# Optimization experiments

Hardware: AMD Instinct MI355X
Metric: run time of the kernel (lower is better)

Reference implementation:

```python
import jax, jax.numpy as jnp
import numpy as np

B, N = 16, 512            # graphs per batch, nodes per graph
V, D_EMB = 100000, 64     # embedding table
F0 = 64                   # raw node feature width
H = 8                     # heads per layer
F_IN0 = F0 + D_EMB + 3    # 131 after concat(emb)+concat(user_emb)
O1, O2 = 128, 128         # f_out of layer 0 and 1
F_IN1 = H * O1            # 1024
EPS = 1e-5


def _xavier(key, shape):
    fan_in, fan_out = shape[-2], shape[-1]
    lim = float(np.sqrt(6.0 / (fan_in + fan_out)))
    return jax.random.uniform(key, shape, jnp.float32, -lim, lim)


def setup_inputs() -> dict:
    key = jax.random.key(0)
    ks = jax.random.split(key, 16)
    vertices = jax.random.randint(ks[0], (B, N), 0, V)
    adj = (jax.random.uniform(ks[1], (B, N, N)) < 0.1).astype(jnp.float32)
    adj = jnp.maximum(adj, jnp.eye(N, dtype=jnp.float32))  # self-loops: no empty softmax rows
    h = jax.random.normal(ks[2], (B, N, F0), jnp.float32)
    user_emb = jax.random.normal(ks[3], (B, N, 3), jnp.float32)
    emb_table = jax.random.normal(ks[4], (V, D_EMB), jnp.float32)
    return {
        "vertices": vertices, "adj": adj, "h": h, "user_emb": user_emb,
        "emb_table": emb_table,
        "norm1_w": jnp.ones((D_EMB,), jnp.float32), "norm1_b": jnp.zeros((D_EMB,), jnp.float32),
        "norm2_w": jnp.ones((3,), jnp.float32), "norm2_b": jnp.zeros((3,), jnp.float32),
        "w0": _xavier(ks[5], (H, F_IN0, O1)),
        "a_src0": _xavier(ks[6], (H, O1, 1)), "a_dst0": _xavier(ks[7], (H, O1, 1)),
        "w1": _xavier(ks[8], (H, F_IN1, O2)),
        "a_src1": _xavier(ks[9], (H, O2, 1)), "a_dst1": _xavier(ks[10], (H, O2, 1)),
    }


def _instance_norm(x, w, b):
    # torch InstanceNorm1d on x.transpose(1,2): normalize over node dim per (batch, channel)
    mu = jnp.mean(x, axis=1, keepdims=True)
    var = jnp.var(x, axis=1, keepdims=True)  # biased variance, as torch
    return (x - mu) * jax.lax.rsqrt(var + EPS) * w + b


def _gat_layer(h, adj, w, a_src, a_dst):
    # h: [b,n,f_in], w: [h,f_in,o]
    hp = jnp.einsum('bnf,hfo->bhno', h, w)            # h_prime
    t = jnp.tanh(hp)
    s = jnp.einsum('bhno,ho->bhn', t, a_src[..., 0])  # attn_src
    d = jnp.einsum('bhno,ho->bhn', t, a_dst[..., 0])  # attn_dst
    attn = s[:, :, :, None] + d[:, :, None, :]        # [b,h,n,n]
    attn = jnp.where(attn >= 0, attn, 0.2 * attn)     # leaky_relu(0.2)
    attn = jnp.where(adj[:, None, :, :] > 0, attn, -jnp.inf)
    attn = jax.nn.softmax(attn, axis=-1)              # (dropout is identity in eval)
    return jnp.einsum('bhnm,bhmo->bhno', attn, hp)


def reference(vertices, adj, h, user_emb, emb_table,
              norm1_w, norm1_b, norm2_w, norm2_b,
              w0, a_src0, a_dst0, w1, a_src1, a_dst1):
    emb = emb_table[vertices]                         # [b,n,D_EMB]
    emb = _instance_norm(emb, norm1_w, norm1_b)
    x = jnp.concatenate([h, emb], axis=2)
    ue = _instance_norm(user_emb, norm2_w, norm2_b)
    x = jnp.concatenate([x, ue], axis=2)              # [b,n,F_IN0]
    # layer 0 (not last): elu + head concat
    x = _gat_layer(x, adj, w0, a_src0, a_dst0)        # [b,H,n,O1]
    x = jax.nn.elu(jnp.transpose(x, (0, 2, 1, 3)).reshape(B, N, H * O1))
    # layer 1 (last): mean over heads
    x = _gat_layer(x, adj, w1, a_src1, a_dst1)        # [b,H,n,O2]
    x = jnp.mean(x, axis=1)                           # [b,n,O2]
    return jax.nn.log_softmax(x, axis=-1)
```

## Files before the change

### kernel.cpp

```cpp
#include <hip/hip_runtime.h>
#include <hip/hip_bf16.h>
#include <cmath>

#define B_  16
#define N_  512
#define H_  8
#define F0_ 64
#define DEMB_ 64
#define FIN0_ 131
#define KP0_ 192
#define O_  128
#define FIN1_ 1024

typedef __attribute__((ext_vector_type(4))) float f32x4;
typedef __attribute__((ext_vector_type(8))) short bf16x8;

__device__ inline ushort f2bf(float f) {
    union { float f; unsigned u; } x; x.f = f;
    unsigned r = x.u + 0x7fff + ((x.u >> 16) & 1);
    return (ushort)(r >> 16);
}
__device__ inline float bf2f(ushort u) {
    union { unsigned u; float f; } x; x.u = ((unsigned)u) << 16;
    return x.f;
}
__device__ inline float tanh_fast(float x) {
    x = fminf(fmaxf(x, -15.f), 15.f);
    float e = __expf(2.f * x);
    return (e - 1.f) * __frcp_rn(e + 1.f);
}

__global__ __launch_bounds__(256) void k_copy_h(const float* __restrict__ h,
                                                ushort* __restrict__ x0) {
    int i = blockIdx.x * 256 + threadIdx.x;
    int r = i >> 6, c = i & 63;
    x0[(size_t)r * KP0_ + c] = f2bf(h[i]);
    x0[(size_t)r * KP0_ + 128 + c] = 0;
}

__global__ __launch_bounds__(256) void k_emb_norm(const int* __restrict__ verts,
                                                  const float* __restrict__ table,
                                                  const float* __restrict__ w,
                                                  const float* __restrict__ bb,
                                                  ushort* __restrict__ x0) {
    int b = blockIdx.x >> 6, c = blockIdx.x & 63;
    int t = threadIdx.x;
    float vals[2], sum = 0.f, sq = 0.f;
#pragma unroll
    for (int i = 0; i < 2; ++i) {
        int n = t + i * 256;
        int vid = verts[b * N_ + n];
        float v = table[(size_t)vid * DEMB_ + c];
        vals[i] = v; sum += v; sq += v * v;
    }
    __shared__ float s0[256], s1[256];
    s0[t] = sum; s1[t] = sq; __syncthreads();
    for (int o = 128; o > 0; o >>= 1) {
        if (t < o) { s0[t] += s0[t + o]; s1[t] += s1[t + o]; }
        __syncthreads();
    }
    float mu = s0[0] * (1.f / N_);
    float var = s1[0] * (1.f / N_) - mu * mu;
    float inv = rsqrtf(var + 1e-5f);
    float ww = w[c], bv = bb[c];
#pragma unroll
    for (int i = 0; i < 2; ++i) {
        int n = t + i * 256;
        x0[((size_t)b * N_ + n) * KP0_ + 64 + c] = f2bf((vals[i] - mu) * inv * ww + bv);
    }
}

__global__ __launch_bounds__(256) void k_ue_norm(const float* __restrict__ ue,
                                                 const float* __restrict__ w,
                                                 const float* __restrict__ bb,
                                                 ushort* __restrict__ x0) {
    int b = blockIdx.x / 3, c = blockIdx.x % 3;
    int t = threadIdx.x;
    float vals[2], sum = 0.f, sq = 0.f;
#pragma unroll
    for (int i = 0; i < 2; ++i) {
        int n = t + i * 256;
        float v = ue[((size_t)b * N_ + n) * 3 + c];
        vals[i] = v; sum += v; sq += v * v;
    }
    __shared__ float s0[256], s1[256];
    s0[t] = sum; s1[t] = sq; __syncthreads();
    for (int o = 128; o > 0; o >>= 1) {
        if (t < o) { s0[t] += s0[t + o]; s1[t] += s1[t + o]; }
        __syncthreads();
    }
    float mu = s0[0] * (1.f / N_);
    float var = s1[0] * (1.f / N_) - mu * mu;
    float inv = rsqrtf(var + 1e-5f);
    float ww = w[c], bv = bb[c];
#pragma unroll
    for (int i = 0; i < 2; ++i) {
        int n = t + i * 256;
        x0[((size_t)b * N_ + n) * KP0_ + 128 + c] = f2bf((vals[i] - mu) * inv * ww + bv);
    }
}

template <int K, int Kp>
__global__ __launch_bounds__(128) void k_wt(const float* __restrict__ w,
                                            ushort* __restrict__ wt) {
    int hh = blockIdx.x / (Kp / 8);
    int kc = blockIdx.x % (Kp / 8);
    int o = threadIdx.x;
    bf16x8 v;
#pragma unroll
    for (int j = 0; j < 8; ++j) {
        int k = kc * 8 + j;
        float f = (k < K) ? w[((size_t)hh * K + k) * 128 + o] : 0.f;
        v[j] = (short)f2bf(f);
    }
    *(bf16x8*)(wt + ((size_t)(hh * 128 + o)) * Kp + kc * 8) = v;
}

__global__ __launch_bounds__(256) void k_mask(const float* __restrict__ adj,
                                              unsigned long long* __restrict__ mask) {
    int gid = blockIdx.x * 256 + threadIdx.x;
    float v = adj[gid];
    unsigned long long m = __ballot(v > 0.f);
    if ((threadIdx.x & 63) == 0) mask[gid >> 6] = m;
}

template <int K>
__global__ __launch_bounds__(256) void k_gemm(const ushort* __restrict__ A,
                                              const ushort* __restrict__ Wt,
                                              const float* __restrict__ asrc,
                                              const float* __restrict__ adst,
                                              ushort* __restrict__ hpT,
                                              float* __restrict__ sout,
                                              float* __restrict__ dout) {
    __shared__ ushort As[128 * 64];
    __shared__ ushort Bs[128 * 64];
    int bid = blockIdx.x;
    int hh = bid & 7;
    int mt = bid >> 3;
    int tid = threadIdx.x;
    int wid = tid >> 6, l = tid & 63;
    int wm = wid >> 1, wn = wid & 1;

    const ushort* Ab = A + (size_t)mt * 128 * K;
    const ushort* Wb = Wt + (size_t)hh * 128 * K;

    f32x4 acc[4][4];
#pragma unroll
    for (int m = 0; m < 4; ++m)
#pragma unroll
        for (int n = 0; n < 4; ++n) acc[m][n] = (f32x4){0.f, 0.f, 0.f, 0.f};

    int srow = tid >> 3;
    int segp = tid & 7;

    for (int kt = 0; kt < K / 64; ++kt) {
        int k0 = kt * 64;
#pragma unroll
        for (int it = 0; it < 4; ++it) {
            int row = it * 32 + srow;
            int segl = segp ^ (row & 7);
            __builtin_amdgcn_global_load_lds(
                (const __attribute__((address_space(1))) void*)(Ab + (size_t)row * K + k0 + segl * 8),
                (__attribute__((address_space(3))) void*)(As + (it * 32 + wid * 8) * 64),
                16, 0, 0);
            __builtin_amdgcn_global_load_lds(
                (const __attribute__((address_space(1))) void*)(Wb + (size_t)row * K + k0 + segl * 8),
                (__attribute__((address_space(3))) void*)(Bs + (it * 32 + wid * 8) * 64),
                16, 0, 0);
        }
        __syncthreads();

        int lr = l & 15;
        int kg = l >> 4;
#pragma unroll
        for (int kk = 0; kk < 2; ++kk) {
            int segl = kk * 4 + kg;
            bf16x8 a[4], b[4];
#pragma unroll
            for (int m = 0; m < 4; ++m) {
                int row = wm * 64 + m * 16 + lr;
                int sp = segl ^ (row & 7);
                a[m] = *(const bf16x8*)(As + row * 64 + sp * 8);
            }
#pragma unroll
            for (int n = 0; n < 4; ++n) {
                int row = wn * 64 + n * 16 + lr;
                int sp = segl ^ (row & 7);
                b[n] = *(const bf16x8*)(Bs + row * 64 + sp * 8);
            }
#pragma unroll
            for (int m = 0; m < 4; ++m)
#pragma unroll
                for (int n = 0; n < 4; ++n)
                    acc[m][n] = __builtin_amdgcn_mfma_f32_16x16x32_bf16(a[m], b[n], acc[m][n], 0, 0, 0);
        }
        __syncthreads();
    }

    int bb = mt >> 2;
    int n_in_b = (mt & 3) * 128;
    int bh = bb * H_ + hh;
    ushort* Hp = hpT + ((size_t)bh * 128) * 512;
#pragma unroll
    for (int m = 0; m < 4; ++m)
#pragma unroll
        for (int n = 0; n < 4; ++n) {
            int rr = wm * 64 + m * 16 + (l >> 4) * 4;
            int cc = wn * 64 + n * 16 + (l & 15);
            ushort4 v;
            v.x = f2bf(acc[m][n][0]);
            v.y = f2bf(acc[m][n][1]);
            v.z = f2bf(acc[m][n][2]);
            v.w = f2bf(acc[m][n][3]);
            *(ushort4*)(Hp + (size_t)cc * 512 + n_in_b + rr) = v;
        }

    float* sP = (float*)As;
    float* dP = sP + 256;
    float av[4], dv[4];
#pragma unroll
    for (int n = 0; n < 4; ++n) {
        int cc = wn * 64 + n * 16 + (l & 15);
        av[n] = asrc[hh * 128 + cc];
        dv[n] = adst[hh * 128 + cc];
    }
#pragma unroll
    for (int m = 0; m < 4; ++m)
#pragma unroll
        for (int j = 0; j < 4; ++j) {
            float sv = 0.f, dvv = 0.f;
#pragma unroll
            for (int n = 0; n < 4; ++n) {
                float th = tanh_fast(acc[m][n][j]);
                sv += th * av[n];
                dvv += th * dv[n];
            }
#pragma unroll
            for (int off = 1; off < 16; off <<= 1) {
                sv += __shfl_xor(sv, off);
                dvv += __shfl_xor(dvv, off);
            }
            if ((l & 15) == 0) {
                int rr = wm * 64 + m * 16 + (l >> 4) * 4 + j;
                sP[wn * 128 + rr] = sv;
                dP[wn * 128 + rr] = dvv;
            }
        }
    __syncthreads();
    if (tid < 128) {
        sout[(size_t)bh * 512 + n_in_b + tid] = sP[tid] + sP[128 + tid];
    } else {
        int r = tid - 128;
        dout[(size_t)bh * 512 + n_in_b + r] = dP[r] + dP[128 + r];
    }
}

template <bool L0>
__global__ __launch_bounds__(256, 2) void k_attn(const ushort* __restrict__ hpT,
                                                 const float* __restrict__ sbuf,
                                                 const float* __restrict__ dbuf,
                                                 const unsigned* __restrict__ mask32,
                                                 ushort* __restrict__ out) {
    __shared__ ushort Vbuf[128 * 64];
    __shared__ ushort Abuf[128 * 64];
    __shared__ float dsh[512];
    __shared__ float rsh[128];

    int bid = blockIdx.x;
    int xcd = bid & 7, idx = bid >> 3;
    int bh = xcd + 8 * (idx & 15);
    int tile = idx >> 4;
    int b = bh >> 3, hh = bh & 7;
    int n0 = tile * 128;
    int t = threadIdx.x;
    int wid = t >> 6, l = t & 63;
    int wm = wid >> 1, wn = wid & 1;
    int lr = l & 15, kg = l >> 4;

    const ushort* Vb = hpT + (size_t)bh * 128 * 512;

    int row = t >> 1, mh = t & 1;
    float sv = sbuf[(size_t)bh * 512 + n0 + row];
    unsigned mw[8];
#pragma unroll
    for (int c = 0; c < 8; ++c)
        mw[c] = mask32[((size_t)(b * 512 + n0 + row) << 4) + c * 2 + mh];

    dsh[t] = dbuf[(size_t)bh * 512 + t];
    dsh[256 + t] = dbuf[(size_t)bh * 512 + 256 + t];
    __syncthreads();

    f32x4 acc[4][4];
#pragma unroll
    for (int m = 0; m < 4; ++m)
#pragma unroll
        for (int n = 0; n < 4; ++n) acc[m][n] = (f32x4){0.f, 0.f, 0.f, 0.f};

    float rsum = 0.f;
    int srow = t >> 3, segp = t & 7;

    for (int c = 0; c < 8; ++c) {
        int m0 = c * 64;
#pragma unroll
        for (int it = 0; it < 4; ++it) {
            int rrow = it * 32 + srow;
            int segl = segp ^ (rrow & 7);
            __builtin_amdgcn_global_load_lds(
                (const __attribute__((address_space(1))) void*)(Vb + (size_t)rrow * 512 + m0 + segl * 8),
                (__attribute__((address_space(3))) void*)(Vbuf + (it * 32 + wid * 8) * 64),
                16, 0, 0);
        }

        const float* dp = dsh + m0 + mh * 32;
        unsigned mwc = mw[c];
#pragma unroll
        for (int j = 0; j < 4; ++j) {
            f32x4 da = *(const f32x4*)(dp + j * 8);
            f32x4 db2 = *(const f32x4*)(dp + j * 8 + 4);
            float ev[8];
#pragma unroll
            for (int q = 0; q < 8; ++q) {
                float dm = (q < 4) ? da[q] : db2[q - 4];
                float lg = sv + dm;
                lg = fmaxf(lg, 0.2f * lg);
                float e = ((mwc >> (j * 8 + q)) & 1) ? __expf(lg) : 0.f;
                rsum += e;
                ev[q] = e;
            }
            unsigned p01, p23, p45, p67;
            asm("v_cvt_pk_bf16_f32 %0, %1, %2" : "=v"(p01) : "v"(ev[0]), "v"(ev[1]));
            asm("v_cvt_pk_bf16_f32 %0, %1, %2" : "=v"(p23) : "v"(ev[2]), "v"(ev[3]));
            asm("v_cvt_pk_bf16_f32 %0, %1, %2" : "=v"(p45) : "v"(ev[4]), "v"(ev[5]));
            asm("v_cvt_pk_bf16_f32 %0, %1, %2" : "=v"(p67) : "v"(ev[6]), "v"(ev[7]));
            int s = mh * 4 + j;
            int phys = s ^ (row & 7);
            uint4 pk4 = {p01, p23, p45, p67};
            *(uint4*)((char*)Abuf + row * 128 + phys * 16) = pk4;
        }
        __syncthreads();

#pragma unroll
        for (int kk = 0; kk < 2; ++kk) {
            int s = kk * 4 + kg;
            bf16x8 a[4], bfr[4];
#pragma unroll
            for (int m = 0; m < 4; ++m) {
                int rw = wm * 64 + m * 16 + lr;
                int sp = s ^ (rw & 7);
                a[m] = *(const bf16x8*)(Vbuf + rw * 64 + sp * 8);
            }
#pragma unroll
            for (int n = 0; n < 4; ++n) {
                int rw = wn * 64 + n * 16 + lr;
                int sp = s ^ (rw & 7);
                bfr[n] = *(const bf16x8*)(Abuf + rw * 64 + sp * 8);
            }
#pragma unroll
            for (int m = 0; m < 4; ++m)
#pragma unroll
                for (int n = 0; n < 4; ++n)
                    acc[m][n] = __builtin_amdgcn_mfma_f32_16x16x32_bf16(a[m], bfr[n], acc[m][n], 0, 0, 0);
        }
        __syncthreads();
    }

    rsum += __shfl_xor(rsum, 1);
    if ((t & 1) == 0) rsh[row] = rsum;
    __syncthreads();

#pragma unroll
    for (int n = 0; n < 4; ++n) {
        int nn = wn * 64 + n * 16 + lr;
        float ri = __frcp_rn(rsh[nn]);
        size_t orow;
        if (L0)
            orow = ((size_t)(b * 512 + n0 + nn)) * FIN1_ + hh * 128;
        else
            orow = ((size_t)bh * 512 + n0 + nn) * 128;
#pragma unroll
        for (int m = 0; m < 4; ++m) {
            int o0 = wm * 64 + m * 16 + kg * 4;
            f32x4 v = acc[m][n];
            ushort4 w;
            float f0 = v[0] * ri, f1 = v[1] * ri, f2 = v[2] * ri, f3 = v[3] * ri;
            if (L0) {
                f0 = (f0 > 0.f) ? f0 : expm1f(f0);
                f1 = (f1 > 0.f) ? f1 : expm1f(f1);
                f2 = (f2 > 0.f) ? f2 : expm1f(f2);
                f3 = (f3 > 0.f) ? f3 : expm1f(f3);
            }
            w.x = f2bf(f0); w.y = f2bf(f1); w.z = f2bf(f2); w.w = f2bf(f3);
            *(ushort4*)(out + orow + o0) = w;
        }
    }
}

__global__ __launch_bounds__(128) void k_out(const ushort* __restrict__ o1,
                                             float* __restrict__ out) {
    int row = blockIdx.x;
    int b = row >> 9, n = row & 511;
    int t = threadIdx.x;
    float v = 0.f;
#pragma unroll
    for (int hh = 0; hh < H_; ++hh)
        v += bf2f(o1[((size_t)(b * H_ + hh) * N_ + n) * O_ + t]);
    v *= 0.125f;
    float m = v;
#pragma unroll
    for (int off = 32; off > 0; off >>= 1) m = fmaxf(m, __shfl_down(m, off));
    __shared__ float red[4];
    if ((t & 63) == 0) red[t >> 6] = m;
    __syncthreads();
    float rm = fmaxf(red[0], red[1]);
    float e = __expf(v - rm);
    float ss = e;
#pragma unroll
    for (int off = 32; off > 0; off >>= 1) ss += __shfl_down(ss, off);
    if ((t & 63) == 0) red[2 + (t >> 6)] = ss;
    __syncthreads();
    float rs2 = red[2] + red[3];
    out[(size_t)row * O_ + t] = v - rm - logf(rs2);
}

extern "C" void kernel_launch(void* const* d_in, const int* in_sizes, int n_in,
                              void* d_out, int out_size, void* d_ws, size_t ws_size,
                              hipStream_t stream) {
    const int*   verts = (const int*)d_in[0];
    const float* adj   = (const float*)d_in[1];
    const float* h     = (const float*)d_in[2];
    const float* ue    = (const float*)d_in[3];
    const float* table = (const float*)d_in[4];
    const float* n1w   = (const float*)d_in[5];
    const float* n1b   = (const float*)d_in[6];
    const float* n2w   = (const float*)d_in[7];
    const float* n2b   = (const float*)d_in[8];
    const float* w0    = (const float*)d_in[9];
    const float* as0   = (const float*)d_in[10];
    const float* ad0   = (const float*)d_in[11];
    const float* w1    = (const float*)d_in[12];
    const float* as1   = (const float*)d_in[13];
    const float* ad1   = (const float*)d_in[14];
    float* out = (float*)d_out;

    ushort* x0p  = (ushort*)d_ws;
    ushort* wt0  = x0p + 1572864;
    ushort* wt1  = wt0 + 196608;
    ushort* hpT  = wt1 + 1048576;
    ushort* x1bf = hpT + 8388608;
    ushort* o1   = x1bf + 8388608;
    unsigned long long* mask = (unsigned long long*)(o1 + 8388608);
    float* sb = (float*)(mask + 65536);
    float* db = sb + 65536;

    hipLaunchKernelGGL(k_copy_h,   dim3(2048), dim3(256), 0, stream, h, x0p);
    hipLaunchKernelGGL(k_emb_norm, dim3(1024), dim3(256), 0, stream, verts, table, n1w, n1b, x0p);
    hipLaunchKernelGGL(k_ue_norm,  dim3(48),   dim3(256), 0, stream, ue, n2w, n2b, x0p);
    hipLaunchKernelGGL((k_wt<FIN0_, KP0_>), dim3(8 * (KP0_ / 8)), dim3(128), 0, stream, w0, wt0);
    hipLaunchKernelGGL((k_wt<FIN1_, FIN1_>), dim3(8 * (FIN1_ / 8)), dim3(128), 0, stream, w1, wt1);
    hipLaunchKernelGGL(k_mask, dim3(16384), dim3(256), 0, stream, adj, mask);

    hipLaunchKernelGGL((k_gemm<KP0_>), dim3(512), dim3(256), 0, stream,
                       x0p, wt0, as0, ad0, hpT, sb, db);
    hipLaunchKernelGGL((k_attn<true>), dim3(512), dim3(256), 0, stream,
                       hpT, sb, db, (const unsigned*)mask, x1bf);

    hipLaunchKernelGGL((k_gemm<FIN1_>), dim3(512), dim3(256), 0, stream,
                       x1bf, wt1, as1, ad1, hpT, sb, db);
    hipLaunchKernelGGL((k_attn<false>), dim3(512), dim3(256), 0, stream,
                       hpT, sb, db, (const unsigned*)mask, o1);

    hipLaunchKernelGGL(k_out, dim3(8192), dim3(128), 0, stream, o1, out);
}
```

Measured before the change: 140.2 us.

## Compute two heads per GEMM block, merge weight transposes, use exp2 with prescaled logits

Each GEMM block now computes two heads from one loaded A tile, so the grid halves and activation tile loads are shared across heads. The cost is double the accumulator registers, with launch bounds asking for two blocks per CU. The two weight-transpose launches are merged into one kernel to save a launch. The attention logits are prescaled by log2(e) in the GEMM epilogue so the attention kernel can call exp2f instead of __expf; leaky-relu commutes with a positive scale, so the softmax result is unchanged.

```diff
diff --git a/kernel.cpp b/kernel.cpp
--- a/kernel.cpp
+++ b/kernel.cpp
@@ -11,6 +11,7 @@
 #define KP0_ 192
 #define O_  128
 #define FIN1_ 1024
+#define LOG2E_ 1.4426950408889634f
 
 typedef __attribute__((ext_vector_type(4))) float f32x4;
 typedef __attribute__((ext_vector_type(8))) short bf16x8;
@@ -100,20 +101,34 @@
     }
 }
 
-template <int K, int Kp>
-__global__ __launch_bounds__(128) void k_wt(const float* __restrict__ w,
-                                            ushort* __restrict__ wt) {
-    int hh = blockIdx.x / (Kp / 8);
-    int kc = blockIdx.x % (Kp / 8);
+__global__ __launch_bounds__(128) void k_wt_all(const float* __restrict__ w0,
+                                                const float* __restrict__ w1,
+                                                ushort* __restrict__ wt0,
+                                                ushort* __restrict__ wt1) {
+    int bid = blockIdx.x;
     int o = threadIdx.x;
-    bf16x8 v;
-#pragma unroll
-    for (int j = 0; j < 8; ++j) {
-        int k = kc * 8 + j;
-        float f = (k < K) ? w[((size_t)hh * K + k) * 128 + o] : 0.f;
-        v[j] = (short)f2bf(f);
-    }
-    *(bf16x8*)(wt + ((size_t)(hh * 128 + o)) * Kp + kc * 8) = v;
+    if (bid < 192) {
+        int hh = bid / 24, kc = bid % 24;
+        bf16x8 v;
+#pragma unroll
+        for (int j = 0; j < 8; ++j) {
+            int k = kc * 8 + j;
+            float f = (k < FIN0_) ? w0[((size_t)hh * FIN0_ + k) * 128 + o] : 0.f;
+            v[j] = (short)f2bf(f);
+        }
+        *(bf16x8*)(wt0 + ((size_t)(hh * 128 + o)) * KP0_ + kc * 8) = v;
+    } else {
+        int b2 = bid - 192;
+        int hh = b2 >> 7, kc = b2 & 127;
+        bf16x8 v;
+#pragma unroll
+        for (int j = 0; j < 8; ++j) {
+            int k = kc * 8 + j;
+            float f = w1[((size_t)hh * FIN1_ + k) * 128 + o];
+            v[j] = (short)f2bf(f);
+        }
+        *(bf16x8*)(wt1 + ((size_t)(hh * 128 + o)) * FIN1_ + kc * 8) = v;
+    }
 }
 
 __global__ __launch_bounds__(256) void k_mask(const float* __restrict__ adj,
@@ -125,30 +140,34 @@
 }
 
 template <int K>
-__global__ __launch_bounds__(256) void k_gemm(const ushort* __restrict__ A,
-                                              const ushort* __restrict__ Wt,
-                                              const float* __restrict__ asrc,
-                                              const float* __restrict__ adst,
-                                              ushort* __restrict__ hpT,
-                                              float* __restrict__ sout,
-                                              float* __restrict__ dout) {
+__global__ __launch_bounds__(256, 2) void k_gemm(const ushort* __restrict__ A,
+                                                 const ushort* __restrict__ Wt,
+                                                 const float* __restrict__ asrc,
+                                                 const float* __restrict__ adst,
+                                                 ushort* __restrict__ hpT,
+                                                 float* __restrict__ sout,
+                                                 float* __restrict__ dout) {
     __shared__ ushort As[128 * 64];
-    __shared__ ushort Bs[128 * 64];
+    __shared__ ushort Bs[2][128 * 64];
     int bid = blockIdx.x;
-    int hh = bid & 7;
-    int mt = bid >> 3;
+    int hp = bid & 3;
+    int mt = bid >> 2;
+    int h0 = hp * 2;
     int tid = threadIdx.x;
     int wid = tid >> 6, l = tid & 63;
     int wm = wid >> 1, wn = wid & 1;
 
     const ushort* Ab = A + (size_t)mt * 128 * K;
-    const ushort* Wb = Wt + (size_t)hh * 128 * K;
-
-    f32x4 acc[4][4];
-#pragma unroll
-    for (int m = 0; m < 4; ++m)
-#pragma unroll
-        for (int n = 0; n < 4; ++n) acc[m][n] = (f32x4){0.f, 0.f, 0.f, 0.f};
+    const ushort* Wb0 = Wt + (size_t)h0 * 128 * K;
+    const ushort* Wb1 = Wb0 + (size_t)128 * K;
+
+    f32x4 acc[2][4][4];
+#pragma unroll
+    for (int hx = 0; hx < 2; ++hx)
+#pragma unroll
+        for (int m = 0; m < 4; ++m)
+#pragma unroll
+            for (int n = 0; n < 4; ++n) acc[hx][m][n] = (f32x4){0.f, 0.f, 0.f, 0.f};
 
     int srow = tid >> 3;
     int segp = tid & 7;
@@ -159,14 +178,17 @@
         for (int it = 0; it < 4; ++it) {
             int row = it * 32 + srow;
             int segl = segp ^ (row & 7);
+            size_t goff = (size_t)row * K + k0 + segl * 8;
+            int loff = (it * 32 + wid * 8) * 64;
             __builtin_amdgcn_global_load_lds(
-                (const __attribute__((address_space(1))) void*)(Ab + (size_t)row * K + k0 + segl * 8),
-                (__attribute__((address_space(3))) void*)(As + (it * 32 + wid * 8) * 64),
-                16, 0, 0);
+                (const __attribute__((address_space(1))) void*)(Ab + goff),
+                (__attribute__((address_space(3))) void*)(As + loff), 16, 0, 0);
             __builtin_amdgcn_global_load_lds(
-                (const __attribute__((address_space(1))) void*)(Wb + (size_t)row * K + k0 + segl * 8),
-                (__attribute__((address_space(3))) void*)(Bs + (it * 32 + wid * 8) * 64),
-                16, 0, 0);
+                (const __attribute__((address_space(1))) void*)(Wb0 + goff),
+                (__attribute__((address_space(3))) void*)(Bs[0] + loff), 16, 0, 0);
+            __builtin_amdgcn_global_load_lds(
+                (const __attribute__((address_space(1))) void*)(Wb1 + goff),
+                (__attribute__((address_space(3))) void*)(Bs[1] + loff), 16, 0, 0);
         }
         __syncthreads();
 
@@ -175,7 +197,7 @@
 #pragma unroll
         for (int kk = 0; kk < 2; ++kk) {
             int segl = kk * 4 + kg;
-            bf16x8 a[4], b[4];
+            bf16x8 a[4], b0[4], b1[4];
 #pragma unroll
             for (int m = 0; m < 4; ++m) {
                 int row = wm * 64 + m * 16 + lr;
@@ -186,72 +208,83 @@
             for (int n = 0; n < 4; ++n) {
                 int row = wn * 64 + n * 16 + lr;
                 int sp = segl ^ (row & 7);
-                b[n] = *(const bf16x8*)(Bs + row * 64 + sp * 8);
+                b0[n] = *(const bf16x8*)(Bs[0] + row * 64 + sp * 8);
+                b1[n] = *(const bf16x8*)(Bs[1] + row * 64 + sp * 8);
             }
 #pragma unroll
             for (int m = 0; m < 4; ++m)
 #pragma unroll
-                for (int n = 0; n < 4; ++n)
-                    acc[m][n] = __builtin_amdgcn_mfma_f32_16x16x32_bf16(a[m], b[n], acc[m][n], 0, 0, 0);
+                for (int n = 0; n < 4; ++n) {
+                    acc[0][m][n] = __builtin_amdgcn_mfma_f32_16x16x32_bf16(a[m], b0[n], acc[0][m][n], 0, 0, 0);
+                    acc[1][m][n] = __builtin_amdgcn_mfma_f32_16x16x32_bf16(a[m], b1[n], acc[1][m][n], 0, 0, 0);
+                }
         }
         __syncthreads();
     }
 
     int bb = mt >> 2;
     int n_in_b = (mt & 3) * 128;
-    int bh = bb * H_ + hh;
-    ushort* Hp = hpT + ((size_t)bh * 128) * 512;
-#pragma unroll
-    for (int m = 0; m < 4; ++m)
-#pragma unroll
-        for (int n = 0; n < 4; ++n) {
-            int rr = wm * 64 + m * 16 + (l >> 4) * 4;
-            int cc = wn * 64 + n * 16 + (l & 15);
-            ushort4 v;
-            v.x = f2bf(acc[m][n][0]);
-            v.y = f2bf(acc[m][n][1]);
-            v.z = f2bf(acc[m][n][2]);
-            v.w = f2bf(acc[m][n][3]);
-            *(ushort4*)(Hp + (size_t)cc * 512 + n_in_b + rr) = v;
-        }
+#pragma unroll
+    for (int hx = 0; hx < 2; ++hx) {
+        int bh = bb * H_ + h0 + hx;
+        ushort* Hp = hpT + ((size_t)bh * 128) * 512;
+#pragma unroll
+        for (int m = 0; m < 4; ++m)
+#pragma unroll
+            for (int n = 0; n < 4; ++n) {
+                int rr = wm * 64 + m * 16 + (l >> 4) * 4;
+                int cc = wn * 64 + n * 16 + (l & 15);
+                ushort4 v;
+                v.x = f2bf(acc[hx][m][n][0]);
+                v.y = f2bf(acc[hx][m][n][1]);
+                v.z = f2bf(acc[hx][m][n][2]);
+                v.w = f2bf(acc[hx][m][n][3]);
+                *(ushort4*)(Hp + (size_t)cc * 512 + n_in_b + rr) = v;
+            }
+    }
 
     float* sP = (float*)As;
     float* dP = sP + 256;
-    float av[4], dv[4];
-#pragma unroll
-    for (int n = 0; n < 4; ++n) {
-        int cc = wn * 64 + n * 16 + (l & 15);
-        av[n] = asrc[hh * 128 + cc];
-        dv[n] = adst[hh * 128 + cc];
-    }
-#pragma unroll
-    for (int m = 0; m < 4; ++m)
-#pragma unroll
-        for (int j = 0; j < 4; ++j) {
-            float sv = 0.f, dvv = 0.f;
-#pragma unroll
-            for (int n = 0; n < 4; ++n) {
-                float th = tanh_fast(acc[m][n][j]);
-                sv += th * av[n];
-                dvv += th * dv[n];
-            }
-#pragma unroll
-            for (int off = 1; off < 16; off <<= 1) {
-                sv += __shfl_xor(sv, off);
-                dvv += __shfl_xor(dvv, off);
-            }
-            if ((l & 15) == 0) {
-                int rr = wm * 64 + m * 16 + (l >> 4) * 4 + j;
-                sP[wn * 128 + rr] = sv;
-                dP[wn * 128 + rr] = dvv;
-            }
-        }
-    __syncthreads();
-    if (tid < 128) {
-        sout[(size_t)bh * 512 + n_in_b + tid] = sP[tid] + sP[128 + tid];
-    } else {
-        int r = tid - 128;
-        dout[(size_t)bh * 512 + n_in_b + r] = dP[r] + dP[128 + r];
+    for (int hx = 0; hx < 2; ++hx) {
+        int hh = h0 + hx;
+        int bh = bb * H_ + hh;
+        float av[4], dv[4];
+#pragma unroll
+        for (int n = 0; n < 4; ++n) {
+            int cc = wn * 64 + n * 16 + (l & 15);
+            av[n] = asrc[hh * 128 + cc];
+            dv[n] = adst[hh * 128 + cc];
+        }
+#pragma unroll
+        for (int m = 0; m < 4; ++m)
+#pragma unroll
+            for (int j = 0; j < 4; ++j) {
+                float sv = 0.f, dvv = 0.f;
+#pragma unroll
+                for (int n = 0; n < 4; ++n) {
+                    float th = tanh_fast(acc[hx][m][n][j]);
+                    sv += th * av[n];
+                    dvv += th * dv[n];
+                }
+#pragma unroll
+                for (int off = 1; off < 16; off <<= 1) {
+                    sv += __shfl_xor(sv, off);
+                    dvv += __shfl_xor(dvv, off);
+                }
+                if ((l & 15) == 0) {
+                    int rr = wm * 64 + m * 16 + (l >> 4) * 4 + j;
+                    sP[wn * 128 + rr] = sv;
+                    dP[wn * 128 + rr] = dvv;
+                }
+            }
+        __syncthreads();
+        if (tid < 128) {
+            sout[(size_t)bh * 512 + n_in_b + tid] = (sP[tid] + sP[128 + tid]) * LOG2E_;
+        } else if (tid < 256) {
+            int r = tid - 128;
+            dout[(size_t)bh * 512 + n_in_b + r] = (dP[r] + dP[128 + r]) * LOG2E_;
+        }
+        __syncthreads();
     }
 }
 
@@ -323,7 +356,7 @@
                 float dm = (q < 4) ? da[q] : db2[q - 4];
                 float lg = sv + dm;
                 lg = fmaxf(lg, 0.2f * lg);
-                float e = ((mwc >> (j * 8 + q)) & 1) ? __expf(lg) : 0.f;
+                float e = ((mwc >> (j * 8 + q)) & 1) ? exp2f(lg) : 0.f;
                 rsum += e;
                 ev[q] = e;
             }
@@ -455,16 +488,15 @@
     hipLaunchKernelGGL(k_copy_h,   dim3(2048), dim3(256), 0, stream, h, x0p);
     hipLaunchKernelGGL(k_emb_norm, dim3(1024), dim3(256), 0, stream, verts, table, n1w, n1b, x0p);
     hipLaunchKernelGGL(k_ue_norm,  dim3(48),   dim3(256), 0, stream, ue, n2w, n2b, x0p);
-    hipLaunchKernelGGL((k_wt<FIN0_, KP0_>), dim3(8 * (KP0_ / 8)), dim3(128), 0, stream, w0, wt0);
-    hipLaunchKernelGGL((k_wt<FIN1_, FIN1_>), dim3(8 * (FIN1_ / 8)), dim3(128), 0, stream, w1, wt1);
-    hipLaunchKernelGGL(k_mask, dim3(16384), dim3(256), 0, stream, adj, mask);
-
-    hipLaunchKernelGGL((k_gemm<KP0_>), dim3(512), dim3(256), 0, stream,
+    hipLaunchKernelGGL(k_wt_all,   dim3(1216), dim3(128), 0, stream, w0, w1, wt0, wt1);
+    hipLaunchKernelGGL(k_mask,     dim3(16384), dim3(256), 0, stream, adj, mask);
+
+    hipLaunchKernelGGL((k_gemm<KP0_>), dim3(256), dim3(256), 0, stream,
                        x0p, wt0, as0, ad0, hpT, sb, db);
     hipLaunchKernelGGL((k_attn<true>), dim3(512), dim3(256), 0, stream,
                        hpT, sb, db, (const unsigned*)mask, x1bf);
 
-    hipLaunchKernelGGL((k_gemm<FIN1_>), dim3(512), dim3(256), 0, stream,
+    hipLaunchKernelGGL((k_gemm<FIN1_>), dim3(256), dim3(256), 0, stream,
                        x1bf, wt1, as1, ad1, hpT, sb, db);
     hipLaunchKernelGGL((k_attn<false>), dim3(512), dim3(256), 0, stream,
                        hpT, sb, db, (const unsigned*)mask, o1);
```

Result: slower. 250.0 us (+78.3%).
